# Kernel tuning notes

Measured on AMD Instinct MI355X. Metric: run time of the kernel, lower is better.

Reference implementation:

```python
import jax, jax.numpy as jnp
import numpy as np

B, C, H, W = 8, 3, 1024, 1024
N_SPOTS = int(H * W * 0.015)  # 15728, matches torch: n = int(H*W*0.015)
KSIZE, SIGMA = 5, 1.5
RMAX = 3  # max snow-box radius (torch.randint(1, 4))


def setup_inputs() -> dict:
    key = jax.random.key(0)
    k1, k2, k3, k4 = jax.random.split(key, 4)
    x = jax.random.uniform(k1, (B, C, H, W), dtype=jnp.float32)
    ys = jax.random.randint(k2, (B, N_SPOTS), 0, H)
    xs = jax.random.randint(k3, (B, N_SPOTS), 0, W)
    rs = jax.random.randint(k4, (B, N_SPOTS), 0, 3)  # radius = rs + 1 in {1,2,3}
    return {"x": x, "ys": ys, "xs": xs, "rs": rs}


def _snow_mask(ys, xs, rs, h, w):
    # Union of axis-aligned boxes: pixel (py,px) is snow iff some spot has
    # |py - y| <= r and |px - x| <= r (box clipping to the image is equivalent).
    b, n = ys.shape
    r = rs + 1  # radii 1..3
    d = jnp.arange(-RMAX, RMAX + 1)
    dy = jnp.repeat(d, 2 * RMAX + 1)  # [49]
    dx = jnp.tile(d, 2 * RMAX + 1)    # [49]
    yy = ys[:, :, None] + dy  # [B, n, 49]
    xx = xs[:, :, None] + dx
    valid = ((jnp.abs(dy) <= r[:, :, None]) & (jnp.abs(dx) <= r[:, :, None])
             & (yy >= 0) & (yy < h) & (xx >= 0) & (xx < w))
    yy = jnp.where(valid, yy, h)  # out-of-bounds sentinel -> dropped by scatter
    xx = jnp.where(valid, xx, w)
    b_idx = jnp.broadcast_to(jnp.arange(b)[:, None, None], yy.shape)
    mask = jnp.zeros((b, h, w), dtype=bool)
    mask = mask.at[b_idx, yy, xx].set(True, mode="drop")
    return mask


def _gauss_kernel():
    coords = jnp.arange(KSIZE, dtype=jnp.float32) - KSIZE // 2
    g = jnp.exp(-coords ** 2 / (2.0 * SIGMA ** 2))
    g = g / g.sum()
    return jnp.outer(g, g)  # [5, 5]


def reference(x, ys, xs, rs):
    b, c, h, w = x.shape
    mask = _snow_mask(ys, xs, rs, h, w)                   # [B, H, W]
    out = jnp.where(mask[:, None, :, :], jnp.float32(0.95), x)
    kernel = jnp.broadcast_to(_gauss_kernel(), (c, 1, KSIZE, KSIZE))  # depthwise OIHW
    pad = KSIZE // 2
    out = jax.lax.conv_general_dilated(
        out, kernel, window_strides=(1, 1), padding=[(pad, pad), (pad, pad)],
        dimension_numbers=("NCHW", "OIHW", "NCHW"), feature_group_count=c)
    return jnp.clip(out, 0.0, 1.0)
```

## Files before the change

kernel.cpp:

```cpp
#include <hip/hip_runtime.h>

#define BB 8
#define CC 3
#define HH 1024
#define WW 1024
#define NS 15728

#define G0 0.1200784f
#define G1 0.2338808f
#define G2 0.2920816f

#define NSTRIPE 16
#define STRW 64

__global__ __launch_bounds__(256) void snow_mask_kernel(
    const int* __restrict__ ys, const int* __restrict__ xs,
    const int* __restrict__ rs, unsigned int* __restrict__ mbits) {
  __shared__ unsigned int lm[HH * 2];
  const int b = blockIdx.y;
  const int sx0 = blockIdx.x * STRW;
  const int tid = threadIdx.x;

  for (int i = tid; i < HH * 2; i += 256) lm[i] = 0u;
  __syncthreads();

  for (int s = tid; s < NS; s += 256) {
    int idx = b * NS + s;
    int y = ys[idx];
    int x = xs[idx];
    int r = rs[idx] + 1;
    int x0 = max(x - r, sx0), x1 = min(x + r, sx0 + (STRW - 1));
    if (x0 > x1) continue;
    int y0 = max(y - r, 0), y1 = min(y + r, HH - 1);
    int lx0 = x0 - sx0, lx1 = x1 - sx0;
    int w0 = lx0 >> 5, w1 = lx1 >> 5;
    unsigned m0 = 0xFFFFFFFFu << (lx0 & 31);
    unsigned m1 = 0xFFFFFFFFu >> (31 - (lx1 & 31));
    if (w0 == w1) {
      unsigned m = m0 & m1;
      for (int py = y0; py <= y1; ++py) atomicOr(&lm[(py << 1) + w0], m);
    } else {
      for (int py = y0; py <= y1; ++py) {
        atomicOr(&lm[(py << 1) + 0], m0);
        atomicOr(&lm[(py << 1) + 1], m1);
      }
    }
  }
  __syncthreads();

  unsigned int* dst = mbits + (((unsigned)(b * HH)) << 5) + blockIdx.x * 2;
  for (int i = tid; i < HH * 2; i += 256) {
    dst[((i >> 1) << 5) + (i & 1)] = lm[i];
  }
}

#define RROWS 16

__global__ __launch_bounds__(256, 6) void snow_blur_kernel(
    const float* __restrict__ x, const unsigned int* __restrict__ mbits,
    float* __restrict__ out) {
  const int bz = blockIdx.y;
  const int b = bz / CC;
  const int gy0 = blockIdx.x * RROWS;
  const int tid = threadIdx.x;
  const int col = tid << 2;

  const float* __restrict__ xp = x + (size_t)bz * (HH * WW);
  const unsigned int* __restrict__ mb = mbits + (((unsigned)(b * HH)) << 5);

  const int colLc = max(col - 4, 0);
  const int colRc = min(col + 4, WW - 4);
  const unsigned loob16 = (col == 0) ? 16u : 0u;
  const unsigned roob16 = (col == WW - 4) ? 16u : 0u;
  const int mwL = colLc >> 5, shL = colLc & 31;
  const int s5 = col & 31;
  const int mwR = colRc >> 5, shR = colRc & 31;

  auto loadrow = [&](int gy, float4& A, float4& Bv, float4& Cv,
                     unsigned& wl, unsigned& wr, unsigned& ro) {
    int gyc = min(max(gy, 0), HH - 1);
    ro = (gy != gyc) ? 16u : 0u;
    const float* rp = xp + ((size_t)gyc << 10);
    const unsigned* mrow = mb + (gyc << 5);
    A = *(const float4*)(rp + colLc);
    Bv = *(const float4*)(rp + col);
    Cv = *(const float4*)(rp + colRc);
    wl = mrow[mwL];
    wr = mrow[mwR];
  };

  auto fix4 = [](float4 v, unsigned m) {
    float4 t;
    t.x = (m & 1u) ? 0.95f : v.x;
    t.y = (m & 2u) ? 0.95f : v.y;
    t.z = (m & 4u) ? 0.95f : v.z;
    t.w = (m & 8u) ? 0.95f : v.w;
    if (m & 16u) { t.x = 0.f; t.y = 0.f; t.z = 0.f; t.w = 0.f; }
    return t;
  };

  auto hrow = [&](float4 A, float4 Bv, float4 Cv,
                  unsigned wl, unsigned wr, unsigned ro) {
    unsigned wc = (s5 == 0) ? wr : wl;
    unsigned ma = ((wl >> shL) & 0xFu) | ro | loob16;
    unsigned mbm = ((wc >> s5) & 0xFu) | ro;
    unsigned mc = ((wr >> shR) & 0xFu) | ro | roob16;
    float4 fA = fix4(A, ma);
    float4 fB = fix4(Bv, mbm);
    float4 fC = fix4(Cv, mc);
    float4 h;
    h.x = G0 * (fA.z + fB.z) + G1 * (fA.w + fB.y) + G2 * fB.x;
    h.y = G0 * (fA.w + fB.w) + G1 * (fB.x + fB.z) + G2 * fB.y;
    h.z = G0 * (fB.x + fC.x) + G1 * (fB.y + fB.w) + G2 * fB.z;
    h.w = G0 * (fB.y + fC.y) + G1 * (fB.z + fC.x) + G2 * fB.w;
    return h;
  };

  float4 h0, h1, h2, h3, h4;
  {
    float4 A, Bv, Cv; unsigned wl, wr, ro;
    loadrow(gy0 - 2, A, Bv, Cv, wl, wr, ro); h0 = hrow(A, Bv, Cv, wl, wr, ro);
    loadrow(gy0 - 1, A, Bv, Cv, wl, wr, ro); h1 = hrow(A, Bv, Cv, wl, wr, ro);
    loadrow(gy0 + 0, A, Bv, Cv, wl, wr, ro); h2 = hrow(A, Bv, Cv, wl, wr, ro);
    loadrow(gy0 + 1, A, Bv, Cv, wl, wr, ro); h3 = hrow(A, Bv, Cv, wl, wr, ro);
  }
  float4 cA, cB, cC; unsigned cwl, cwr, cro;
  loadrow(gy0 + 2, cA, cB, cC, cwl, cwr, cro);

  float* op = out + (size_t)bz * (HH * WW) + ((size_t)gy0 << 10) + col;
#pragma unroll
  for (int k = 0; k < RROWS; ++k) {
    float4 nA, nB, nC; unsigned nwl, nwr, nro;
    loadrow(gy0 + k + 3, nA, nB, nC, nwl, nwr, nro);

    h4 = hrow(cA, cB, cC, cwl, cwr, cro);

    float4 s;
    s.x = G0 * (h0.x + h4.x) + G1 * (h1.x + h3.x) + G2 * h2.x;
    s.y = G0 * (h0.y + h4.y) + G1 * (h1.y + h3.y) + G2 * h2.y;
    s.z = G0 * (h0.z + h4.z) + G1 * (h1.z + h3.z) + G2 * h2.z;
    s.w = G0 * (h0.w + h4.w) + G1 * (h1.w + h3.w) + G2 * h2.w;
    s.x = fminf(fmaxf(s.x, 0.f), 1.f);
    s.y = fminf(fmaxf(s.y, 0.f), 1.f);
    s.z = fminf(fmaxf(s.z, 0.f), 1.f);
    s.w = fminf(fmaxf(s.w, 0.f), 1.f);
    *(float4*)op = s;
    op += WW;

    h0 = h1; h1 = h2; h2 = h3; h3 = h4;
    cA = nA; cB = nB; cC = nC; cwl = nwl; cwr = nwr; cro = nro;
  }
}

extern "C" void kernel_launch(void* const* d_in, const int* in_sizes, int n_in,
                              void* d_out, int out_size, void* d_ws, size_t ws_size,
                              hipStream_t stream) {
  const float* x = (const float*)d_in[0];
  const int* ys = (const int*)d_in[1];
  const int* xs = (const int*)d_in[2];
  const int* rs = (const int*)d_in[3];
  float* out = (float*)d_out;

  unsigned int* mbits = (unsigned int*)d_ws;

  dim3 mgrid(NSTRIPE, BB);
  snow_mask_kernel<<<mgrid, 256, 0, stream>>>(ys, xs, rs, mbits);

  dim3 grid(HH / RROWS, BB * CC);
  snow_blur_kernel<<<grid, 256, 0, stream>>>(x, mbits, out);
}
```

Measured before the change: 252.5 us.

## Trim halo loads, prefetch deeper, and narrow snow-mask stripes with vectorized spot reads

The blur kernel now loads only float2 halos (two columns each side) instead of full float4 neighbours. It combines two mask words into a 64-bit value to pull out the needed bits, and prefetches three rows ahead instead of one, with the occupancy hint lowered from 6 to 4 blocks. The mask kernel uses 32-column stripes, one word per row, which doubles the block count and removes the two-word branch. It reads spot coordinates as int4 with software prefetch. The aim is to cut load traffic and latency stalls, at the cost of more registers per thread and less occupancy.

```diff
diff --git a/kernel.cpp b/kernel.cpp
--- a/kernel.cpp
+++ b/kernel.cpp
@@ -5,58 +5,69 @@
 #define HH 1024
 #define WW 1024
 #define NS 15728
+#define NG (NS / 4)
 
 #define G0 0.1200784f
 #define G1 0.2338808f
 #define G2 0.2920816f
 
-#define NSTRIPE 16
-#define STRW 64
+#define NSTRIPE 32
 
 __global__ __launch_bounds__(256) void snow_mask_kernel(
     const int* __restrict__ ys, const int* __restrict__ xs,
     const int* __restrict__ rs, unsigned int* __restrict__ mbits) {
-  __shared__ unsigned int lm[HH * 2];
+  __shared__ unsigned int lm[HH];
   const int b = blockIdx.y;
-  const int sx0 = blockIdx.x * STRW;
+  const int sx0 = blockIdx.x << 5;
   const int tid = threadIdx.x;
 
-  for (int i = tid; i < HH * 2; i += 256) lm[i] = 0u;
+  for (int i = tid; i < HH; i += 256) lm[i] = 0u;
   __syncthreads();
 
-  for (int s = tid; s < NS; s += 256) {
-    int idx = b * NS + s;
-    int y = ys[idx];
-    int x = xs[idx];
-    int r = rs[idx] + 1;
-    int x0 = max(x - r, sx0), x1 = min(x + r, sx0 + (STRW - 1));
-    if (x0 > x1) continue;
+  const int4* __restrict__ y4 = (const int4*)(ys + b * NS);
+  const int4* __restrict__ x4 = (const int4*)(xs + b * NS);
+  const int4* __restrict__ r4 = (const int4*)(rs + b * NS);
+
+  auto spot = [&](int y, int x, int r) {
+    r += 1;
+    int x0 = max(x - r, sx0), x1 = min(x + r, sx0 + 31);
+    if (x0 > x1) return;
     int y0 = max(y - r, 0), y1 = min(y + r, HH - 1);
-    int lx0 = x0 - sx0, lx1 = x1 - sx0;
-    int w0 = lx0 >> 5, w1 = lx1 >> 5;
-    unsigned m0 = 0xFFFFFFFFu << (lx0 & 31);
-    unsigned m1 = 0xFFFFFFFFu >> (31 - (lx1 & 31));
-    if (w0 == w1) {
-      unsigned m = m0 & m1;
-      for (int py = y0; py <= y1; ++py) atomicOr(&lm[(py << 1) + w0], m);
-    } else {
-      for (int py = y0; py <= y1; ++py) {
-        atomicOr(&lm[(py << 1) + 0], m0);
-        atomicOr(&lm[(py << 1) + 1], m1);
-      }
-    }
+    unsigned m = (0xFFFFFFFFu << (x0 & 31)) & (0xFFFFFFFFu >> (31 - (x1 & 31)));
+    for (int py = y0; py <= y1; ++py) atomicOr(&lm[py], m);
+  };
+
+  int g = tid;
+  int4 Y = {0, 0, 0, 0}, X = {0, 0, 0, 0}, R = {0, 0, 0, 0};
+  bool have = g < NG;
+  if (have) { Y = y4[g]; X = x4[g]; R = r4[g]; }
+  while (have) {
+    int gn = g + 256;
+    int4 Yn = {0, 0, 0, 0}, Xn = {0, 0, 0, 0}, Rn = {0, 0, 0, 0};
+    bool haven = gn < NG;
+    if (haven) { Yn = y4[gn]; Xn = x4[gn]; Rn = r4[gn]; }
+    spot(Y.x, X.x, R.x);
+    spot(Y.y, X.y, R.y);
+    spot(Y.z, X.z, R.z);
+    spot(Y.w, X.w, R.w);
+    g = gn; Y = Yn; X = Xn; R = Rn; have = haven;
   }
   __syncthreads();
 
-  unsigned int* dst = mbits + (((unsigned)(b * HH)) << 5) + blockIdx.x * 2;
-  for (int i = tid; i < HH * 2; i += 256) {
-    dst[((i >> 1) << 5) + (i & 1)] = lm[i];
-  }
+  unsigned int* dst = mbits + ((unsigned)(b * HH) << 5) + blockIdx.x;
+  for (int i = tid; i < HH; i += 256) dst[i << 5] = lm[i];
 }
 
 #define RROWS 16
 
-__global__ __launch_bounds__(256, 6) void snow_blur_kernel(
+struct Row {
+  float4 B;
+  float2 L;
+  float2 R;
+  unsigned m0, m1;
+};
+
+__global__ __launch_bounds__(256, 4) void snow_blur_kernel(
     const float* __restrict__ x, const unsigned int* __restrict__ mbits,
     float* __restrict__ out) {
   const int bz = blockIdx.y;
@@ -66,74 +77,79 @@
   const int col = tid << 2;
 
   const float* __restrict__ xp = x + (size_t)bz * (HH * WW);
-  const unsigned int* __restrict__ mb = mbits + (((unsigned)(b * HH)) << 5);
+  const unsigned int* __restrict__ mb = mbits + ((unsigned)(b * HH) << 5);
 
-  const int colLc = max(col - 4, 0);
-  const int colRc = min(col + 4, WW - 4);
-  const unsigned loob16 = (col == 0) ? 16u : 0u;
-  const unsigned roob16 = (col == WW - 4) ? 16u : 0u;
-  const int mwL = colLc >> 5, shL = colLc & 31;
-  const int s5 = col & 31;
-  const int mwR = colRc >> 5, shR = colRc & 31;
+  const int cL = max(col - 2, 0);
+  const int cR = min(col + 4, WW - 2);
+  const unsigned loob = (col == 0) ? 16u : 0u;
+  const unsigned roob = (col == WW - 4) ? 16u : 0u;
+  const int w = cL >> 5;
+  const int w2 = min(w + 1, 31);
+  const int bpL = cL - (w << 5);
+  const int bpB = col - (w << 5);
+  const int bpR = col + 4 - (w << 5);
 
-  auto loadrow = [&](int gy, float4& A, float4& Bv, float4& Cv,
-                     unsigned& wl, unsigned& wr, unsigned& ro) {
+  auto loadrow = [&](int gy, Row& rw) {
     int gyc = min(max(gy, 0), HH - 1);
-    ro = (gy != gyc) ? 16u : 0u;
     const float* rp = xp + ((size_t)gyc << 10);
     const unsigned* mrow = mb + (gyc << 5);
-    A = *(const float4*)(rp + colLc);
-    Bv = *(const float4*)(rp + col);
-    Cv = *(const float4*)(rp + colRc);
-    wl = mrow[mwL];
-    wr = mrow[mwR];
+    rw.B = *(const float4*)(rp + col);
+    rw.L = *(const float2*)(rp + cL);
+    rw.R = *(const float2*)(rp + cR);
+    rw.m0 = mrow[w];
+    rw.m1 = mrow[w2];
   };
 
-  auto fix4 = [](float4 v, unsigned m) {
-    float4 t;
-    t.x = (m & 1u) ? 0.95f : v.x;
-    t.y = (m & 2u) ? 0.95f : v.y;
-    t.z = (m & 4u) ? 0.95f : v.z;
-    t.w = (m & 8u) ? 0.95f : v.w;
-    if (m & 16u) { t.x = 0.f; t.y = 0.f; t.z = 0.f; t.w = 0.f; }
-    return t;
-  };
-
-  auto hrow = [&](float4 A, float4 Bv, float4 Cv,
-                  unsigned wl, unsigned wr, unsigned ro) {
-    unsigned wc = (s5 == 0) ? wr : wl;
-    unsigned ma = ((wl >> shL) & 0xFu) | ro | loob16;
-    unsigned mbm = ((wc >> s5) & 0xFu) | ro;
-    unsigned mc = ((wr >> shR) & 0xFu) | ro | roob16;
-    float4 fA = fix4(A, ma);
-    float4 fB = fix4(Bv, mbm);
-    float4 fC = fix4(Cv, mc);
+  auto consume = [&](const Row& rw, unsigned ro) {
+    unsigned long long mw =
+        (unsigned long long)rw.m0 | ((unsigned long long)rw.m1 << 32);
+    unsigned bL = ((unsigned)(mw >> bpL) & 3u) | ro | loob;
+    unsigned bB = ((unsigned)(mw >> bpB) & 0xFu) | ro;
+    unsigned bR = ((unsigned)(mw >> bpR) & 3u) | ro | roob;
+    float2 fL;
+    fL.x = (bL & 1u) ? 0.95f : rw.L.x;
+    fL.y = (bL & 2u) ? 0.95f : rw.L.y;
+    if (bL & 16u) { fL.x = 0.f; fL.y = 0.f; }
+    float4 fB;
+    fB.x = (bB & 1u) ? 0.95f : rw.B.x;
+    fB.y = (bB & 2u) ? 0.95f : rw.B.y;
+    fB.z = (bB & 4u) ? 0.95f : rw.B.z;
+    fB.w = (bB & 8u) ? 0.95f : rw.B.w;
+    if (bB & 16u) { fB.x = 0.f; fB.y = 0.f; fB.z = 0.f; fB.w = 0.f; }
+    float2 fR;
+    fR.x = (bR & 1u) ? 0.95f : rw.R.x;
+    fR.y = (bR & 2u) ? 0.95f : rw.R.y;
+    if (bR & 16u) { fR.x = 0.f; fR.y = 0.f; }
     float4 h;
-    h.x = G0 * (fA.z + fB.z) + G1 * (fA.w + fB.y) + G2 * fB.x;
-    h.y = G0 * (fA.w + fB.w) + G1 * (fB.x + fB.z) + G2 * fB.y;
-    h.z = G0 * (fB.x + fC.x) + G1 * (fB.y + fB.w) + G2 * fB.z;
-    h.w = G0 * (fB.y + fC.y) + G1 * (fB.z + fC.x) + G2 * fB.w;
+    h.x = G0 * (fL.x + fB.z) + G1 * (fL.y + fB.y) + G2 * fB.x;
+    h.y = G0 * (fL.y + fB.w) + G1 * (fB.x + fB.z) + G2 * fB.y;
+    h.z = G0 * (fB.x + fR.x) + G1 * (fB.y + fB.w) + G2 * fB.z;
+    h.w = G0 * (fB.y + fR.y) + G1 * (fB.z + fR.x) + G2 * fB.w;
     return h;
   };
 
-  float4 h0, h1, h2, h3, h4;
-  {
-    float4 A, Bv, Cv; unsigned wl, wr, ro;
-    loadrow(gy0 - 2, A, Bv, Cv, wl, wr, ro); h0 = hrow(A, Bv, Cv, wl, wr, ro);
-    loadrow(gy0 - 1, A, Bv, Cv, wl, wr, ro); h1 = hrow(A, Bv, Cv, wl, wr, ro);
-    loadrow(gy0 + 0, A, Bv, Cv, wl, wr, ro); h2 = hrow(A, Bv, Cv, wl, wr, ro);
-    loadrow(gy0 + 1, A, Bv, Cv, wl, wr, ro); h3 = hrow(A, Bv, Cv, wl, wr, ro);
-  }
-  float4 cA, cB, cC; unsigned cwl, cwr, cro;
-  loadrow(gy0 + 2, cA, cB, cC, cwl, cwr, cro);
+  auto rof = [&](int gy) { return (gy < 0 || gy >= HH) ? 16u : 0u; };
+
+  Row p0, p1, p2, p3, s0, s1, s2;
+  loadrow(gy0 - 2, p0);
+  loadrow(gy0 - 1, p1);
+  loadrow(gy0 + 0, p2);
+  loadrow(gy0 + 1, p3);
+  loadrow(gy0 + 2, s0);
+  loadrow(gy0 + 3, s1);
+  loadrow(gy0 + 4, s2);
+  float4 h0 = consume(p0, rof(gy0 - 2));
+  float4 h1 = consume(p1, rof(gy0 - 1));
+  float4 h2 = consume(p2, 0u);
+  float4 h3 = consume(p3, 0u);
 
   float* op = out + (size_t)bz * (HH * WW) + ((size_t)gy0 << 10) + col;
 #pragma unroll
   for (int k = 0; k < RROWS; ++k) {
-    float4 nA, nB, nC; unsigned nwl, nwr, nro;
-    loadrow(gy0 + k + 3, nA, nB, nC, nwl, nwr, nro);
+    Row nr{};
+    if (k < RROWS - 3) loadrow(gy0 + 5 + k, nr);
 
-    h4 = hrow(cA, cB, cC, cwl, cwr, cro);
+    float4 h4 = consume(s0, rof(gy0 + 2 + k));
 
     float4 s;
     s.x = G0 * (h0.x + h4.x) + G1 * (h1.x + h3.x) + G2 * h2.x;
@@ -147,8 +163,8 @@
     *(float4*)op = s;
     op += WW;
 
+    s0 = s1; s1 = s2; s2 = nr;
     h0 = h1; h1 = h2; h2 = h3; h3 = h4;
-    cA = nA; cB = nB; cC = nC; cwl = nwl; cwr = nwr; cro = nro;
   }
 }
 
```

Result: faster. 205.4 us (-18.6%).
